# Kernel tuning notes

Hardware: AMD Instinct MI355X
Metric: run time of the kernel (lower is better)

## Reference

```python
import jax, jax.numpy as jnp
import numpy as np


def _patch_desc(x, patch_size):
    # x: (n, c, h, w). Replicate-pad by patch_size//2 and gather all
    # patch_size*patch_size shifted views -> (n, c*p*p, h*w) descriptors.
    n, c, h, w = x.shape
    step = patch_size // 2
    y = jnp.pad(x, ((0, 0), (0, 0), (step, step), (step, step)), mode='edge')
    feats = [y[:, :, i:i + h, j:j + w]
             for i in range(patch_size) for j in range(patch_size)]
    d = jnp.stack(feats, axis=2)            # (n, c, p*p, h, w)
    return d.reshape(n, c * patch_size * patch_size, h * w)


def setup_inputs() -> dict:
    key = jax.random.key(0)
    k1, k2 = jax.random.split(key)
    n, c, h, w = 4, 16, 64, 64
    s = jax.random.normal(k1, (n, c, h, w), dtype=jnp.float32)
    t = jax.random.normal(k2, (n, c, h, w), dtype=jnp.float32)
    return {"s": s, "t": t, "patch_size": 3}


def reference(s, t, patch_size):
    n, c, h, w = s.shape
    q = _patch_desc(s, patch_size)          # (n, d, hw) source queries
    p = _patch_desc(t, patch_size)          # (n, d, hw) target points
    # Squared-L2 nearest neighbor per source patch (exact version of FLANN kNN)
    qn = jnp.sum(q * q, axis=1)             # (n, hw)
    pn = jnp.sum(p * p, axis=1)             # (n, hw)
    cross = jnp.einsum('ndi,ndj->nij', q, p)  # (n, hw_q, hw_t)
    d2 = qn[:, :, None] - 2.0 * cross + pn[:, None, :]
    idx = jnp.argmin(d2, axis=2)            # (n, hw) flat target index
    nnd = jnp.min(d2, axis=2)               # (n, hw) squared distance
    idy = idx // w
    idx_x = idx % w
    nnf = jnp.stack([idy.reshape(n, h, w), idx_x.reshape(n, h, w)], axis=1)
    nnd = nnd.reshape(n, 1, h, w)
    return nnf.astype(jnp.int32), nnd
```

## Files before the change

kernel.cpp:

```cpp
#include <hip/hip_runtime.h>


#define N_  4
#define C_  16
#define H_  64
#define W_  64
#define HW_ 4096
#define K_  160
#define SPLITS_M 8
#define KKSTRIDE 528

#define SPLITS_V 4
#define TILES_PER_SPLIT_V 4

typedef _Float16 f16;
typedef _Float16 f16x8 __attribute__((ext_vector_type(8)));
typedef float    f32x4 __attribute__((ext_vector_type(4)));

__device__ __forceinline__ int iclamp(int v, int lo, int hi) {
    return v < lo ? lo : (v > hi ? hi : v);
}

__device__ __forceinline__ void async_ld16(const void* g, void* l) {
    __builtin_amdgcn_global_load_lds(
        (const __attribute__((address_space(1))) unsigned int*)g,
        (__attribute__((address_space(3))) unsigned int*)l, 16, 0, 0);
}

__global__ __launch_bounds__(256)
void build_desc_norms_kernel(const float* __restrict__ s,
                             const float* __restrict__ t,
                             f16* __restrict__ Qh, f16* __restrict__ Ql,
                             f16* __restrict__ Ph, f16* __restrict__ Pl,
                             float* __restrict__ pn,
                             float* __restrict__ qn) {
    const int y0  = blockIdx.x;
    const int n   = blockIdx.y;
    const int src = blockIdx.z;
    const float* img = (src ? s : t) + n * (C_ * HW_);
    f16* Dh = src ? Qh : Ph;
    f16* Dl = src ? Ql : Pl;
    float* nrm = src ? qn : pn;

    __shared__ float imgS[3][C_][W_];
    __shared__ float nS[4][W_];
    const int tid = threadIdx.x;
    #pragma unroll
    for (int k = 0; k < 12; ++k) {
        const int idx = tid + k * 256;
        const int x = idx & 63, c = (idx >> 6) & 15, r = idx >> 10;
        const int gy = iclamp(y0 + r - 1, 0, H_ - 1);
        imgS[r][c][x] = img[c * HW_ + gy * W_ + x];
    }
    __syncthreads();

    const int q = tid >> 6, x = tid & 63;
    const int pix = y0 * W_ + x;
    float nacc = 0.f;
    #pragma unroll
    for (int u = 0; u < 5; ++u) {
        const int kk = q * 5 + u;
        f16x8 hv, lv;
        if (kk < 18) {
            const int d  = kk >> 1;
            const int c0 = (kk & 1) * 8;
            const int dy = (d * 11) >> 5;
            const int dx = d - dy * 3;
            const int xs = iclamp(x + dx - 1, 0, W_ - 1);
            #pragma unroll
            for (int cc = 0; cc < 8; ++cc) {
                const float v = imgS[dy][c0 + cc][xs];
                const f16 h = (f16)v;
                hv[cc] = h;
                lv[cc] = (f16)(v - (float)h);
                nacc += v * v;
            }
        } else {
            #pragma unroll
            for (int cc = 0; cc < 8; ++cc) { hv[cc] = (f16)0.f; lv[cc] = (f16)0.f; }
        }
        const size_t off = ((size_t)(n * 20 + kk) * HW_ + pix) * 8;
        *(f16x8*)&Dh[off] = hv;
        *(f16x8*)&Dl[off] = lv;
    }
    nS[q][x] = nacc;
    __syncthreads();
    if (tid < W_)
        nrm[n * HW_ + pix] = nS[0][tid] + nS[1][tid] + nS[2][tid] + nS[3][tid];
}

__global__ __launch_bounds__(256, 2)
void mfma_nn_kernel(const f16* __restrict__ Qh, const f16* __restrict__ Ql,
                    const f16* __restrict__ Ph, const f16* __restrict__ Pl,
                    const float* __restrict__ pn_g,
                    unsigned long long* __restrict__ partial) {
    const int bid   = blockIdx.x;
    const int split = bid & 7;
    const int n     = (bid >> 3) & 3;
    const int iblk  = bid >> 5;
    const int tid  = threadIdx.x;
    const int wave = tid >> 6, lane = tid & 63;
    const int m = lane & 15, quad = lane >> 4;
    const int irow0 = iblk * 256 + wave * 64;

    __shared__ f16 B0[20 * KKSTRIDE];
    __shared__ f16 B1[20 * KKSTRIDE];
    __shared__ float pnS[512];

    f16x8 Ah[4][5], Al[4][5];
    #pragma unroll
    for (int is = 0; is < 4; ++is)
        #pragma unroll
        for (int kc = 0; kc < 5; ++kc) {
            const size_t off = ((size_t)(n * 20 + kc * 4 + quad) * HW_ +
                                irow0 + is * 16 + m) * 8;
            Ah[is][kc] = *(const f16x8*)(Qh + off);
            Al[is][kc] = *(const f16x8*)(Ql + off);
        }

    const int jsplit0 = split * 512;
    pnS[tid]       = pn_g[n * HW_ + jsplit0 + tid];
    pnS[tid + 256] = pn_g[n * HW_ + jsplit0 + tid + 256];

    float    bd[4][4];
    unsigned bj[4][4];
    #pragma unroll
    for (int is = 0; is < 4; ++is)
        #pragma unroll
        for (int rg = 0; rg < 4; ++rg) { bd[is][rg] = 3.0e38f; bj[is][rg] = 0u; }

    const int skk  = wave * 5;
    const int sarr = lane >> 5;
    const int srow = lane & 31;
    const f16* sbase = sarr ? Pl : Ph;

    #define STAGE(BUF, T)                                                     \
        {   _Pragma("unroll")                                                 \
            for (int u = 0; u < 5; ++u) {                                     \
                const int kk = skk + u;                                       \
                const f16* g = sbase + ((size_t)(n * 20 + kk) * HW_ +         \
                                        jsplit0 + (T) * 32 + srow) * 8;       \
                async_ld16(g, (void*)&BUF[kk * KKSTRIDE + lane * 8]);         \
            }                                                                 \
        }

    #define COMPUTE(BUF, T)                                                   \
        {   _Pragma("unroll")                                                 \
            for (int js = 0; js < 2; ++js) {                                  \
                f32x4 Cf[4];                                                  \
                _Pragma("unroll")                                             \
                for (int is = 0; is < 4; ++is)                                \
                    Cf[is] = (f32x4){0.f, 0.f, 0.f, 0.f};                     \
                _Pragma("unroll")                                             \
                for (int kc = 0; kc < 5; ++kc) {                              \
                    const int kb = (kc * 4 + quad) * KKSTRIDE +               \
                                   (js * 16 + m) * 8;                         \
                    const f16x8 bh = *(const f16x8*)&BUF[kb];                 \
                    const f16x8 bl = *(const f16x8*)&BUF[kb + 256];           \
                    _Pragma("unroll")                                         \
                    for (int is = 0; is < 4; ++is) {                          \
                        Cf[is] = __builtin_amdgcn_mfma_f32_16x16x32_f16(      \
                            Ah[is][kc], bh, Cf[is], 0, 0, 0);                 \
                        Cf[is] = __builtin_amdgcn_mfma_f32_16x16x32_f16(      \
                            Al[is][kc], bh, Cf[is], 0, 0, 0);                 \
                        Cf[is] = __builtin_amdgcn_mfma_f32_16x16x32_f16(      \
                            Ah[is][kc], bl, Cf[is], 0, 0, 0);                 \
                    }                                                         \
                }                                                             \
                const int jloc = (T) * 32 + js * 16 + m;                      \
                const float pnv = pnS[jloc];                                  \
                _Pragma("unroll")                                             \
                for (int is = 0; is < 4; ++is)                                \
                    _Pragma("unroll")                                         \
                    for (int rg = 0; rg < 4; ++rg) {                          \
                        const float d = fmaf(Cf[is][rg], -2.f, pnv);          \
                        if (d < bd[is][rg]) {       \
                            bd[is][rg] = d;                                   \
                            bj[is][rg] = (unsigned)jloc;                      \
                        }                                                     \
                    }                                                         \
            }                                                                 \
        }

    STAGE(B0, 0)
    asm volatile("s_waitcnt vmcnt(0)" ::: "memory");
    __syncthreads();

    for (int jt = 0; jt < 16; jt += 2) {
        if (jt + 1 < 16) STAGE(B1, jt + 1)
        COMPUTE(B0, jt)
        asm volatile("s_waitcnt vmcnt(0)" ::: "memory");
        __syncthreads();
        if (jt + 2 < 16) STAGE(B0, jt + 2)
        COMPUTE(B1, jt + 1)
        asm volatile("s_waitcnt vmcnt(0)" ::: "memory");
        __syncthreads();
    }
    #undef STAGE
    #undef COMPUTE

    #pragma unroll
    for (int is = 0; is < 4; ++is)
        #pragma unroll
        for (int rg = 0; rg < 4; ++rg) {
            float    d = bd[is][rg];
            unsigned j = (unsigned)jsplit0 + bj[is][rg];
            #pragma unroll
            for (int off = 1; off < 16; off <<= 1) {
                const float    od = __shfl_xor(d, off, 64);
                const unsigned oj = __shfl_xor(j, off, 64);
                const bool take = (od < d) || (od == d && oj < j);
                d = take ? od : d;
                j = take ? oj : j;
            }
            if (m == 0) {
                const int i = irow0 + is * 16 + quad * 4 + rg;
                partial[(size_t)(split * N_ + n) * HW_ + i] =
                    ((unsigned long long)j << 32) |
                    (unsigned long long)__float_as_uint(d);
            }
        }
}

__global__ __launch_bounds__(256)
void finalize_mfma_kernel(const unsigned long long* __restrict__ partial,
                          const float* __restrict__ qn_g,
                          float* __restrict__ out) {
    const int id  = blockIdx.x * 256 + threadIdx.x;
    const int n   = id >> 12;
    const int pix = id & 4095;
    float    bd = 3.0e38f;
    unsigned bj = 0u;
    #pragma unroll
    for (int sp = 0; sp < SPLITS_M; ++sp) {
        const unsigned long long v = partial[(size_t)(sp * N_ + n) * HW_ + pix];
        const float    d = __uint_as_float((unsigned)(v & 0xffffffffull));
        const unsigned j = (unsigned)(v >> 32);
        const bool take = (d < bd) || (d == bd && j < bj);
        bd = take ? d : bd;
        bj = take ? j : bj;
    }
    out[n * 2 * HW_ + pix]            = (float)(bj >> 6);
    out[n * 2 * HW_ + HW_ + pix]      = (float)(bj & 63);
    out[N_ * 2 * HW_ + n * HW_ + pix] = bd + qn_g[n * HW_ + pix];
}

__global__ __launch_bounds__(256)
void prep_norms_kernel(const float* __restrict__ s,
                       const float* __restrict__ t,
                       float* __restrict__ pn,
                       float* __restrict__ qn) {
    const int gid   = blockIdx.x * 256 + threadIdx.x;
    const int which = gid >> 14;
    const int id    = gid & 16383;
    const int n     = id >> 12;
    const int pix   = id & 4095;
    const int y = pix >> 6, x = pix & 63;
    const float* base = (which ? s : t) + n * (C_ * HW_);
    float acc = 0.f;
    for (int c = 0; c < C_; ++c) {
        const float* bc = base + c * HW_;
        #pragma unroll
        for (int dy = 0; dy < 3; ++dy) {
            const float* br = bc + iclamp(y + dy - 1, 0, H_ - 1) * W_;
            #pragma unroll
            for (int dx = 0; dx < 3; ++dx) {
                float v = br[iclamp(x + dx - 1, 0, W_ - 1)];
                acc += v * v;
            }
        }
    }
    (which ? qn : pn)[id] = acc;
}

__global__ __launch_bounds__(256)
void patchmatch_main_kernel(const float* __restrict__ s,
                            const float* __restrict__ t,
                            const float* __restrict__ pn_g,
                            const float* __restrict__ qn_g,
                            unsigned long long* __restrict__ partial) {
    const int yq    = blockIdx.x;
    const int n     = blockIdx.y;
    const int split = blockIdx.z;
    const int tid  = threadIdx.x;
    const int tx   = tid & 15;
    const int ty   = tid >> 4;
    const int i0   = ty * 4;
    const int jrow = tx >> 2;
    const int jx0  = (tx & 3) * 16;

    __shared__ float qS[C_][3][68];
    __shared__ float tS[C_][6][68];
    __shared__ float qnS[W_];

    const float* sb = s + n * (C_ * HW_);
    const float* tb = t + n * (C_ * HW_);

    #pragma unroll
    for (int k = 0; k < 3; ++k) {
        const int id = tid + k * 256;
        const int sg = id & 15;
        const int c  = (id >> 4) & 15;
        const int r  = id >> 8;
        const int gr = iclamp(yq + r - 1, 0, H_ - 1);
        const float4 v = *(const float4*)&sb[c * HW_ + gr * W_ + sg * 4];
        float* dst = &qS[c][r][1 + sg * 4];
        dst[0] = v.x; dst[1] = v.y; dst[2] = v.z; dst[3] = v.w;
    }
    if (tid < 48) {
        const int c  = tid & 15;
        const int r  = tid >> 4;
        const int gr = iclamp(yq + r - 1, 0, H_ - 1);
        qS[c][r][0]  = sb[c * HW_ + gr * W_];
        qS[c][r][65] = sb[c * HW_ + gr * W_ + 63];
    }
    if (tid < W_) qnS[tid] = qn_g[n * HW_ + yq * W_ + tid];

    unsigned long long best[4] = {~0ull, ~0ull, ~0ull, ~0ull};

    for (int ytl = 0; ytl < TILES_PER_SPLIT_V; ++ytl) {
        const int yt = split * TILES_PER_SPLIT_V + ytl;
        __syncthreads();
        #pragma unroll
        for (int k = 0; k < 6; ++k) {
            const int id = tid + k * 256;
            const int sg = id & 15;
            const int c  = (id >> 4) & 15;
            const int r  = id >> 8;
            const int gr = iclamp(4 * yt + r - 1, 0, H_ - 1);
            const float4 v = *(const float4*)&tb[c * HW_ + gr * W_ + sg * 4];
            float* dst = &tS[c][r][1 + sg * 4];
            dst[0] = v.x; dst[1] = v.y; dst[2] = v.z; dst[3] = v.w;
        }
        if (tid < 96) {
            const int c  = tid & 15;
            const int r  = tid >> 4;
            const int gr = iclamp(4 * yt + r - 1, 0, H_ - 1);
            tS[c][r][0]  = tb[c * HW_ + gr * W_];
            tS[c][r][65] = tb[c * HW_ + gr * W_ + 63];
        }
        __syncthreads();

        float acc[4][16];
        #pragma unroll
        for (int a = 0; a < 4; ++a)
            #pragma unroll
            for (int b = 0; b < 16; ++b) acc[a][b] = 0.f;

        for (int c = 0; c < C_; ++c) {
            #pragma unroll
            for (int dy = 0; dy < 3; ++dy) {
                float qv[6], tv[18];
                *(float4*)&qv[0] = *(const float4*)&qS[c][dy][i0];
                *(float2*)&qv[4] = *(const float2*)&qS[c][dy][i0 + 4];
                const float* trow = &tS[c][jrow + dy][jx0];
                *(float4*)&tv[0]  = *(const float4*)&trow[0];
                *(float4*)&tv[4]  = *(const float4*)&trow[4];
                *(float4*)&tv[8]  = *(const float4*)&trow[8];
                *(float4*)&tv[12] = *(const float4*)&trow[12];
                *(float2*)&tv[16] = *(const float2*)&trow[16];
                #pragma unroll
                for (int dx = 0; dx < 3; ++dx)
                    #pragma unroll
                    for (int a = 0; a < 4; ++a)
                        #pragma unroll
                        for (int b = 0; b < 16; ++b)
                            acc[a][b] += qv[a + dx] * tv[b + dx];
            }
        }

        const int jbase = yt * 256 + jrow * W_ + jx0;
        float pnv[16];
        const float* png = &pn_g[n * HW_ + jbase];
        *(float4*)&pnv[0]  = *(const float4*)&png[0];
        *(float4*)&pnv[4]  = *(const float4*)&png[4];
        *(float4*)&pnv[8]  = *(const float4*)&png[8];
        *(float4*)&pnv[12] = *(const float4*)&png[12];
        #pragma unroll
        for (int a = 0; a < 4; ++a) {
            const float qn = qnS[i0 + a];
            #pragma unroll
            for (int b = 0; b < 16; ++b) {
                const float d2 = qn + pnv[b] - 2.f * acc[a][b];
                unsigned long long cand =
                    ((unsigned long long)__float_as_uint(d2) << 32) |
                    (unsigned)(jbase + b);
                best[a] = cand < best[a] ? cand : best[a];
            }
        }
    }

    #pragma unroll
    for (int a = 0; a < 4; ++a) {
        unsigned long long v = best[a];
        #pragma unroll
        for (int mm = 8; mm >= 1; mm >>= 1) {
            unsigned long long o = __shfl_xor(v, mm, 64);
            v = o < v ? o : v;
        }
        best[a] = v;
    }
    if (tx == 0) {
        #pragma unroll
        for (int a = 0; a < 4; ++a)
            partial[((split * N_ + n) * HW_) + yq * W_ + i0 + a] = best[a];
    }
}

__global__ __launch_bounds__(256)
void finalize_kernel(const unsigned long long* __restrict__ partial,
                     float* __restrict__ out) {
    const int id  = blockIdx.x * 256 + threadIdx.x;
    const int n   = id >> 12;
    const int pix = id & 4095;
    unsigned long long best = ~0ull;
    #pragma unroll
    for (int sp = 0; sp < SPLITS_V; ++sp) {
        unsigned long long v = partial[(sp * N_ + n) * HW_ + pix];
        best = v < best ? v : best;
    }
    const unsigned j = (unsigned)(best & 0xffffffffu);
    const float d2 = __uint_as_float((unsigned)(best >> 32));
    out[n * 2 * HW_ + pix]            = (float)(j >> 6);
    out[n * 2 * HW_ + HW_ + pix]      = (float)(j & 63);
    out[N_ * 2 * HW_ + n * HW_ + pix] = d2;
}

__global__ __launch_bounds__(256)
void patchmatch_mono_kernel(const float* __restrict__ s,
                            const float* __restrict__ t,
                            float* __restrict__ out) {
    const int yq  = blockIdx.x;
    const int n   = blockIdx.y;
    const int tid = threadIdx.x;
    const int tx  = tid & 15;
    const int ty  = tid >> 4;
    const int i0  = ty * 4;
    const int jrow = tx >> 3;
    const int jx0  = (tx & 7) * 8;

    __shared__ float qS[C_][3][68];
    __shared__ float tS[C_][4][68];
    __shared__ float pnS[HW_];
    __shared__ float qnS[W_];

    const float* sb = s + n * (C_ * HW_);
    const float* tb = t + n * (C_ * HW_);

    for (int jj = tid; jj < HW_; jj += 256) {
        const int y = jj >> 6, x = jj & 63;
        float acc = 0.f;
        for (int c = 0; c < C_; ++c) {
            const float* tc = tb + c * HW_;
            #pragma unroll
            for (int dy = 0; dy < 3; ++dy) {
                const float* tr = tc + iclamp(y + dy - 1, 0, H_ - 1) * W_;
                #pragma unroll
                for (int dx = 0; dx < 3; ++dx) {
                    float v = tr[iclamp(x + dx - 1, 0, W_ - 1)];
                    acc += v * v;
                }
            }
        }
        pnS[jj] = acc;
    }
    for (int idx = tid; idx < C_ * 3 * 66; idx += 256) {
        const int c   = idx / (3 * 66);
        const int rem = idx - c * (3 * 66);
        const int rr  = rem / 66;
        const int xi  = rem - rr * 66;
        qS[c][rr][xi] = sb[c * HW_ + iclamp(yq + rr - 1, 0, H_ - 1) * W_ +
                           iclamp(xi - 1, 0, W_ - 1)];
    }
    __syncthreads();
    if (tid < W_) {
        float acc = 0.f;
        for (int c = 0; c < C_; ++c)
            #pragma unroll
            for (int dy = 0; dy < 3; ++dy)
                #pragma unroll
                for (int dx = 0; dx < 3; ++dx) {
                    float v = qS[c][dy][tid + dx];
                    acc += v * v;
                }
        qnS[tid] = acc;
    }

    unsigned long long best[4] = {~0ull, ~0ull, ~0ull, ~0ull};
    for (int yt = 0; yt < 32; ++yt) {
        __syncthreads();
        for (int idx = tid; idx < C_ * 4 * 66; idx += 256) {
            const int c   = idx / (4 * 66);
            const int rem = idx - c * (4 * 66);
            const int rr  = rem / 66;
            const int xi  = rem - rr * 66;
            tS[c][rr][xi] = tb[c * HW_ + iclamp(2 * yt + rr - 1, 0, H_ - 1) * W_ +
                               iclamp(xi - 1, 0, W_ - 1)];
        }
        __syncthreads();

        float acc[4][8];
        #pragma unroll
        for (int a = 0; a < 4; ++a)
            #pragma unroll
            for (int b = 0; b < 8; ++b) acc[a][b] = 0.f;

        for (int c = 0; c < C_; ++c) {
            #pragma unroll
            for (int dy = 0; dy < 3; ++dy) {
                float qv[8], tv[12];
                *(float4*)&qv[0] = *(const float4*)&qS[c][dy][i0];
                *(float4*)&qv[4] = *(const float4*)&qS[c][dy][i0 + 4];
                const float* trow = &tS[c][jrow + dy][jx0];
                *(float4*)&tv[0] = *(const float4*)&trow[0];
                *(float4*)&tv[4] = *(const float4*)&trow[4];
                *(float4*)&tv[8] = *(const float4*)&trow[8];
                #pragma unroll
                for (int dx = 0; dx < 3; ++dx)
                    #pragma unroll
                    for (int a = 0; a < 4; ++a)
                        #pragma unroll
                        for (int b = 0; b < 8; ++b)
                            acc[a][b] += qv[a + dx] * tv[b + dx];
            }
        }
        const int rbase = (2 * yt + jrow) * W_ + jx0;
        #pragma unroll
        for (int a = 0; a < 4; ++a) {
            const float qn = qnS[i0 + a];
            #pragma unroll
            for (int b = 0; b < 8; ++b) {
                const int j = rbase + b;
                const float d2 = qn + pnS[j] - 2.f * acc[a][b];
                unsigned long long cand =
                    ((unsigned long long)__float_as_uint(d2) << 32) | (unsigned)j;
                best[a] = cand < best[a] ? cand : best[a];
            }
        }
    }
    #pragma unroll
    for (int a = 0; a < 4; ++a) {
        unsigned long long v = best[a];
        #pragma unroll
        for (int mm = 8; mm >= 1; mm >>= 1) {
            unsigned long long o = __shfl_xor(v, mm, 64);
            v = o < v ? o : v;
        }
        best[a] = v;
    }
    if (tx == 0) {
        #pragma unroll
        for (int a = 0; a < 4; ++a) {
            const int x = i0 + a;
            const unsigned j = (unsigned)(best[a] & 0xffffffffu);
            const float d2 = __uint_as_float((unsigned)(best[a] >> 32));
            const int pix = yq * W_ + x;
            out[n * 2 * HW_ + pix]            = (float)(j >> 6);
            out[n * 2 * HW_ + HW_ + pix]      = (float)(j & 63);
            out[N_ * 2 * HW_ + n * HW_ + pix] = d2;
        }
    }
}

extern "C" void kernel_launch(void* const* d_in, const int* in_sizes, int n_in,
                              void* d_out, int out_size, void* d_ws, size_t ws_size,
                              hipStream_t stream) {
    const float* s = (const float*)d_in[0];
    const float* t = (const float*)d_in[1];
    float* out = (float*)d_out;

    const size_t norm_b  = (size_t)N_ * HW_ * 4;
    const size_t part_b  = (size_t)SPLITS_M * N_ * HW_ * 8;
    const size_t desc_b  = (size_t)N_ * HW_ * K_ * 2;
    const size_t need_m  = 2 * norm_b + part_b + 4 * desc_b;

    if (ws_size >= need_m) {
        char* w = (char*)d_ws;
        float* pn = (float*)w;                       w += norm_b;
        float* qn = (float*)w;                       w += norm_b;
        unsigned long long* partial = (unsigned long long*)w; w += part_b;
        f16* Qh = (f16*)w;  w += desc_b;
        f16* Ql = (f16*)w;  w += desc_b;
        f16* Ph = (f16*)w;  w += desc_b;
        f16* Pl = (f16*)w;

        build_desc_norms_kernel<<<dim3(64, N_, 2), 256, 0, stream>>>(
            s, t, Qh, Ql, Ph, Pl, pn, qn);
        mfma_nn_kernel<<<512, 256, 0, stream>>>(Qh, Ql, Ph, Pl, pn, partial);
        finalize_mfma_kernel<<<64, 256, 0, stream>>>(partial, qn, out);
        return;
    }

    const size_t need_v = 2 * norm_b + (size_t)SPLITS_V * N_ * HW_ * 8;
    if (ws_size >= need_v) {
        float* pn = (float*)d_ws;
        float* qn = pn + N_ * HW_;
        unsigned long long* partial =
            (unsigned long long*)((char*)d_ws + 2 * norm_b);
        prep_norms_kernel<<<128, 256, 0, stream>>>(s, t, pn, qn);
        dim3 grid(H_, N_, SPLITS_V);
        patchmatch_main_kernel<<<grid, 256, 0, stream>>>(s, t, pn, qn, partial);
        finalize_kernel<<<64, 256, 0, stream>>>(partial, out);
        return;
    }

    dim3 grid(H_, N_);
    patchmatch_mono_kernel<<<grid, 256, 0, stream>>>(s, t, out);
}
```

Measured before the change: 127.2 us.

## Halve per-wave query tile and target tile to double grid parallelism

Each wave now holds 32 query rows instead of 64, and each staged target tile covers 16 columns instead of 32. The grid doubles to 1024 blocks and the loop runs 32 tile steps. The padded LDS stride and the shared norm buffer are dropped, so target norms are read straight from global memory. This aims to raise occupancy and spread work over more CUs. In exchange it lowers MFMA reuse per LDS load, doubles the barrier count, and may bring LDS bank conflicts without the padding.

```diff
diff --git a/kernel.cpp b/kernel.cpp
--- a/kernel.cpp
+++ b/kernel.cpp
@@ -8,7 +8,6 @@
 #define HW_ 4096
 #define K_  160
 #define SPLITS_M 8
-#define KKSTRIDE 528
 
 #define SPLITS_V 4
 #define TILES_PER_SPLIT_V 4
@@ -89,7 +88,7 @@
         nrm[n * HW_ + pix] = nS[0][tid] + nS[1][tid] + nS[2][tid] + nS[3][tid];
 }
 
-__global__ __launch_bounds__(256, 2)
+__global__ __launch_bounds__(256)
 void mfma_nn_kernel(const f16* __restrict__ Qh, const f16* __restrict__ Ql,
                     const f16* __restrict__ Ph, const f16* __restrict__ Pl,
                     const float* __restrict__ pn_g,
@@ -101,15 +100,14 @@
     const int tid  = threadIdx.x;
     const int wave = tid >> 6, lane = tid & 63;
     const int m = lane & 15, quad = lane >> 4;
-    const int irow0 = iblk * 256 + wave * 64;
-
-    __shared__ f16 B0[20 * KKSTRIDE];
-    __shared__ f16 B1[20 * KKSTRIDE];
-    __shared__ float pnS[512];
-
-    f16x8 Ah[4][5], Al[4][5];
-    #pragma unroll
-    for (int is = 0; is < 4; ++is)
+    const int irow0 = iblk * 128 + wave * 32;
+
+    __shared__ f16 B0[640 * 8];
+    __shared__ f16 B1[640 * 8];
+
+    f16x8 Ah[2][5], Al[2][5];
+    #pragma unroll
+    for (int is = 0; is < 2; ++is)
         #pragma unroll
         for (int kc = 0; kc < 5; ++kc) {
             const size_t off = ((size_t)(n * 20 + kc * 4 + quad) * HW_ +
@@ -119,79 +117,75 @@
         }
 
     const int jsplit0 = split * 512;
-    pnS[tid]       = pn_g[n * HW_ + jsplit0 + tid];
-    pnS[tid + 256] = pn_g[n * HW_ + jsplit0 + tid + 256];
-
-    float    bd[4][4];
-    unsigned bj[4][4];
-    #pragma unroll
-    for (int is = 0; is < 4; ++is)
+    const float* png = pn_g + n * HW_ + jsplit0;
+
+    float    bd[2][4];
+    unsigned bj[2][4];
+    #pragma unroll
+    for (int is = 0; is < 2; ++is)
         #pragma unroll
         for (int rg = 0; rg < 4; ++rg) { bd[is][rg] = 3.0e38f; bj[is][rg] = 0u; }
-
-    const int skk  = wave * 5;
-    const int sarr = lane >> 5;
-    const int srow = lane & 31;
-    const f16* sbase = sarr ? Pl : Ph;
 
     #define STAGE(BUF, T)                                                     \
         {   _Pragma("unroll")                                                 \
-            for (int u = 0; u < 5; ++u) {                                     \
-                const int kk = skk + u;                                       \
-                const f16* g = sbase + ((size_t)(n * 20 + kk) * HW_ +         \
-                                        jsplit0 + (T) * 32 + srow) * 8;       \
-                async_ld16(g, (void*)&BUF[kk * KKSTRIDE + lane * 8]);         \
+            for (int it = 0; it < 3; ++it) {                                  \
+                const int c = tid + it * 256;                                 \
+                if (c < 640) {                                                \
+                    const int kk  = c >> 5;                                   \
+                    const int idx = c & 31;                                   \
+                    const int arr = idx >> 4;                                 \
+                    const int row = idx & 15;                                 \
+                    const f16* g = (arr ? Pl : Ph) +                          \
+                        ((size_t)(n * 20 + kk) * HW_ +                        \
+                         jsplit0 + (T) * 16 + row) * 8;                       \
+                    async_ld16(g, (void*)&BUF[c * 8]);                        \
+                }                                                             \
             }                                                                 \
         }
 
     #define COMPUTE(BUF, T)                                                   \
-        {   _Pragma("unroll")                                                 \
-            for (int js = 0; js < 2; ++js) {                                  \
-                f32x4 Cf[4];                                                  \
+        {   f32x4 Cf[2];                                                      \
+            Cf[0] = (f32x4){0.f, 0.f, 0.f, 0.f};                              \
+            Cf[1] = (f32x4){0.f, 0.f, 0.f, 0.f};                              \
+            _Pragma("unroll")                                                 \
+            for (int kc = 0; kc < 5; ++kc) {                                  \
+                const int kb = ((kc * 4 + quad) * 32 + m) * 8;                \
+                const f16x8 bh = *(const f16x8*)&BUF[kb];                     \
+                const f16x8 bl = *(const f16x8*)&BUF[kb + 128];               \
                 _Pragma("unroll")                                             \
-                for (int is = 0; is < 4; ++is)                                \
-                    Cf[is] = (f32x4){0.f, 0.f, 0.f, 0.f};                     \
+                for (int is = 0; is < 2; ++is) {                              \
+                    Cf[is] = __builtin_amdgcn_mfma_f32_16x16x32_f16(          \
+                        Ah[is][kc], bh, Cf[is], 0, 0, 0);                     \
+                    Cf[is] = __builtin_amdgcn_mfma_f32_16x16x32_f16(          \
+                        Al[is][kc], bh, Cf[is], 0, 0, 0);                     \
+                    Cf[is] = __builtin_amdgcn_mfma_f32_16x16x32_f16(          \
+                        Ah[is][kc], bl, Cf[is], 0, 0, 0);                     \
+                }                                                             \
+            }                                                                 \
+            const int jloc = (T) * 16 + m;                                    \
+            const float pnv = png[jloc];                                      \
+            _Pragma("unroll")                                                 \
+            for (int is = 0; is < 2; ++is)                                    \
                 _Pragma("unroll")                                             \
-                for (int kc = 0; kc < 5; ++kc) {                              \
-                    const int kb = (kc * 4 + quad) * KKSTRIDE +               \
-                                   (js * 16 + m) * 8;                         \
-                    const f16x8 bh = *(const f16x8*)&BUF[kb];                 \
-                    const f16x8 bl = *(const f16x8*)&BUF[kb + 256];           \
-                    _Pragma("unroll")                                         \
-                    for (int is = 0; is < 4; ++is) {                          \
-                        Cf[is] = __builtin_amdgcn_mfma_f32_16x16x32_f16(      \
-                            Ah[is][kc], bh, Cf[is], 0, 0, 0);                 \
-                        Cf[is] = __builtin_amdgcn_mfma_f32_16x16x32_f16(      \
-                            Al[is][kc], bh, Cf[is], 0, 0, 0);                 \
-                        Cf[is] = __builtin_amdgcn_mfma_f32_16x16x32_f16(      \
-                            Ah[is][kc], bl, Cf[is], 0, 0, 0);                 \
+                for (int rg = 0; rg < 4; ++rg) {                              \
+                    const float d = fmaf(Cf[is][rg], -2.f, pnv);              \
+                    if (d < bd[is][rg]) {           \
+                        bd[is][rg] = d;                                       \
+                        bj[is][rg] = (unsigned)jloc;                          \
                     }                                                         \
                 }                                                             \
-                const int jloc = (T) * 32 + js * 16 + m;                      \
-                const float pnv = pnS[jloc];                                  \
-                _Pragma("unroll")                                             \
-                for (int is = 0; is < 4; ++is)                                \
-                    _Pragma("unroll")                                         \
-                    for (int rg = 0; rg < 4; ++rg) {                          \
-                        const float d = fmaf(Cf[is][rg], -2.f, pnv);          \
-                        if (d < bd[is][rg]) {       \
-                            bd[is][rg] = d;                                   \
-                            bj[is][rg] = (unsigned)jloc;                      \
-                        }                                                     \
-                    }                                                         \
-            }                                                                 \
         }
 
     STAGE(B0, 0)
     asm volatile("s_waitcnt vmcnt(0)" ::: "memory");
     __syncthreads();
 
-    for (int jt = 0; jt < 16; jt += 2) {
-        if (jt + 1 < 16) STAGE(B1, jt + 1)
+    for (int jt = 0; jt < 32; jt += 2) {
+        if (jt + 1 < 32) STAGE(B1, jt + 1)
         COMPUTE(B0, jt)
         asm volatile("s_waitcnt vmcnt(0)" ::: "memory");
         __syncthreads();
-        if (jt + 2 < 16) STAGE(B0, jt + 2)
+        if (jt + 2 < 32) STAGE(B0, jt + 2)
         COMPUTE(B1, jt + 1)
         asm volatile("s_waitcnt vmcnt(0)" ::: "memory");
         __syncthreads();
@@ -200,7 +194,7 @@
     #undef COMPUTE
 
     #pragma unroll
-    for (int is = 0; is < 4; ++is)
+    for (int is = 0; is < 2; ++is)
         #pragma unroll
         for (int rg = 0; rg < 4; ++rg) {
             float    d = bd[is][rg];
@@ -586,7 +580,7 @@
 
         build_desc_norms_kernel<<<dim3(64, N_, 2), 256, 0, stream>>>(
             s, t, Qh, Ql, Ph, Pl, pn, qn);
-        mfma_nn_kernel<<<512, 256, 0, stream>>>(Qh, Ql, Ph, Pl, pn, partial);
+        mfma_nn_kernel<<<1024, 256, 0, stream>>>(Qh, Ql, Ph, Pl, pn, partial);
         finalize_mfma_kernel<<<64, 256, 0, stream>>>(partial, qn, out);
         return;
     }
```

Measured after the change: 129.0 us. About the same (+1.4%).
